# Optimization experiments

Measured on AMD Instinct MI355X. Metric: run time of the kernel, lower is better.

Reference implementation:

```python
import jax, jax.numpy as jnp
import numpy as np

NUM_SAMPLES = 100  # hard-coded in the original forward


def _bilinear(img, x, y):
    """Bilinear sample img (H,W) at pixel coords x,y (any shape); border padding.
    Matches F.grid_sample(align_corners=True, padding_mode='border') since the
    original normalizes by (W-1)/(H-1) which maps back to the same pixel coords."""
    H, W = img.shape
    x0 = jnp.floor(x); y0 = jnp.floor(y)
    wx = x - x0; wy = y - y0
    x0i = jnp.clip(x0, 0, W - 1).astype(jnp.int32)
    x1i = jnp.clip(x0 + 1, 0, W - 1).astype(jnp.int32)
    y0i = jnp.clip(y0, 0, H - 1).astype(jnp.int32)
    y1i = jnp.clip(y0 + 1, 0, H - 1).astype(jnp.int32)
    return (img[y0i, x0i] * (1 - wx) * (1 - wy)
            + img[y0i, x1i] * wx * (1 - wy)
            + img[y1i, x0i] * (1 - wx) * wy
            + img[y1i, x1i] * wx * wy)


def setup_inputs() -> dict:
    key = jax.random.key(0)
    k1, k2, k3 = jax.random.split(key, 3)
    H = W = 2048
    N = 100000
    distance_image = jax.random.uniform(k1, (H, W), dtype=jnp.float32)
    points = jax.random.uniform(k2, (N, 2), dtype=jnp.float32) * (H - 1)
    normals = jax.random.normal(k3, (N, 2), dtype=jnp.float32)
    return {"distance_image": distance_image, "points": points, "normals": normals}


def reference(distance_image, points, normals):
    H, W = distance_image.shape
    N = points.shape[0]
    # original clamps both coords to [0, max(H-1, W-1)]
    pts = jnp.clip(points, 0.0, float(max(H - 1, W - 1)))  # (N,2)

    # direction perpendicular to normal, normalized
    d = jnp.stack([-normals[:, 1], normals[:, 0]], axis=-1)
    d = d / jnp.linalg.norm(d, axis=-1, keepdims=True)  # (N,2)
    dx, dy = d[:, 0], d[:, 1]
    px, py = pts[:, 0], pts[:, 1]

    maxf = jnp.finfo(d.dtype).max
    sdx = jnp.where(dx != 0, dx, 1.0)
    sdy = jnp.where(dy != 0, dy, 1.0)
    t_left = jnp.where(dx != 0, (0.0 - px) / sdx, -maxf)
    t_right = jnp.where(dx != 0, (W - 1.0 - px) / sdx, maxf)
    t_top = jnp.where(dy != 0, (0.0 - py) / sdy, -maxf)
    t_bottom = jnp.where(dy != 0, (H - 1.0 - py) / sdy, maxf)
    t_min = jnp.maximum(t_left, t_top)
    t_max = jnp.minimum(t_right, t_bottom)

    p1 = pts + t_min[:, None] * d  # (N,2)
    p2 = pts + t_max[:, None] * d  # (N,2)

    ts = jnp.linspace(0.0, 1.0, NUM_SAMPLES, dtype=pts.dtype)  # (S,)
    line = p1[:, None, :] + ts[None, :, None] * (p2 - p1)[:, None, :]  # (N,S,2)
    lx = jnp.clip(line[..., 0], 0.0, W - 1.0)
    ly = jnp.clip(line[..., 1], 0.0, H - 1.0)
    line = jnp.stack([lx, ly], axis=-1)  # clamped sampled points (N,S,2)

    vals = _bilinear(distance_image, lx, ly)  # (N,S)
    ref_val = _bilinear(distance_image, px, py)  # (N,)

    # local minima: strict minimum vs both neighbors, indices shifted by +1
    center = vals[:, 1:-1]
    minima = (center < vals[:, :-2]) & (center < vals[:, 2:])  # (N,S-2)

    # distance from each candidate (interior sample points) to the reference point
    dist = jnp.linalg.norm(line[:, 1:-1, :] - pts[:, None, :], axis=-1)  # (N,S-2)
    dist = jnp.where(minima, dist, jnp.inf)
    nearest = jnp.argmin(dist, axis=1)  # (N,)
    nearest_val = vals[jnp.arange(N), nearest + 1]  # (N,)

    # per-point mse of two scalars, then mean over points
    return jnp.mean((nearest_val - ref_val) ** 2)
```

## Files before the change

kernel.cpp:

```cpp
#include <hip/hip_runtime.h>
#include <float.h>
#include <math.h>

#define NSAMP 100
#define IMG_W 2048
#define IMG_H 2048
#define SEG 25
#define NSEG 4
#define NREG 8

typedef _Float16 h2_t __attribute__((ext_vector_type(2), aligned(4)));
typedef _Float16 h4_t __attribute__((ext_vector_type(4), aligned(8)));
typedef _Float16 h8_t __attribute__((ext_vector_type(8), aligned(16)));

__device__ __forceinline__ float tparam(int s) {
    return (s == NSAMP - 1) ? 1.0f : (float)((double)s * (1.0 / 99.0));
}

__device__ __forceinline__ void chord(float px, float py, float nx, float ny,
                                      float& p1x, float& p1y, float& vx, float& vy) {
    float ddx = -ny, ddy = nx;
    float nrm = sqrtf(ddx * ddx + ddy * ddy);
    float dx = ddx / nrm, dy = ddy / nrm;
    const float maxf = FLT_MAX;
    float sdx = (dx != 0.f) ? dx : 1.f;
    float sdy = (dy != 0.f) ? dy : 1.f;
    float t_left   = (dx != 0.f) ? (0.f    - px) / sdx : -maxf;
    float t_right  = (dx != 0.f) ? (2047.f - px) / sdx :  maxf;
    float t_top    = (dy != 0.f) ? (0.f    - py) / sdy : -maxf;
    float t_bottom = (dy != 0.f) ? (2047.f - py) / sdy :  maxf;
    float t_min = fmaxf(t_left, t_top);
    float t_max = fminf(t_right, t_bottom);
    p1x = px + t_min * dx; p1y = py + t_min * dy;
    float p2x = px + t_max * dx, p2y = py + t_max * dy;
    vx = p2x - p1x; vy = p2y - p1y;
}

__global__ void zero_qcnt_kernel(unsigned int* __restrict__ qcnt) {
    if (threadIdx.x < NREG) qcnt[threadIdx.x] = 0u;
}

__global__ __launch_bounds__(256) void convert_bin_kernel(
        const float* __restrict__ in, h2_t* __restrict__ V,
        const float* __restrict__ points, const float* __restrict__ normals,
        float4* __restrict__ pts4, unsigned int* __restrict__ regs,
        unsigned int* __restrict__ qcnt,
        double* __restrict__ accum, unsigned int* __restrict__ done,
        int N) {
    __shared__ unsigned int lh[NREG];
    if (threadIdx.x < NREG) lh[threadIdx.x] = 0u;
    __syncthreads();
    int idx = blockIdx.x * blockDim.x + threadIdx.x;
    if (idx == 0) { *accum = 0.0; *done = 0u; }

    {
        int y  = idx >> 9;
        int x4 = (idx & 511) << 2;
        int y1 = min(y + 1, IMG_H - 1);
        float4 a = *(const float4*)(in + (size_t)y  * IMG_W + x4);
        float4 b = *(const float4*)(in + (size_t)y1 * IMG_W + x4);
        h8_t o;
        o[0] = (_Float16)a.x; o[1] = (_Float16)b.x;
        o[2] = (_Float16)a.y; o[3] = (_Float16)b.y;
        o[4] = (_Float16)a.z; o[5] = (_Float16)b.z;
        o[6] = (_Float16)a.w; o[7] = (_Float16)b.w;
        *(h8_t*)(V + (size_t)y * IMG_W + x4) = o;
    }

    if (idx < N) {
        float px = fminf(fmaxf(points[2 * idx],     0.f), 2047.f);
        float py = fminf(fmaxf(points[2 * idx + 1], 0.f), 2047.f);
        float nx = normals[2 * idx];
        float ny = normals[2 * idx + 1];
        pts4[idx] = make_float4(px, py, nx, ny);
        float p1x, p1y, vx, vy;
        chord(px, py, nx, ny, p1x, p1y, vx, vy);
        unsigned int packed = 0;
        #pragma unroll
        for (int seg = 0; seg < NSEG; ++seg) {
            int s_begin = SEG * seg;
            int s_end   = min(s_begin + SEG + 1, NSAMP - 1);
            float f = (float)(s_begin + s_end) * 0.5f / 99.0f;
            float mx = fminf(fmaxf(p1x + f * vx, 0.f), 2047.f);
            float my = fminf(fmaxf(p1y + f * vy, 0.f), 2047.f);
            unsigned int r = ((unsigned int)my >> 10) * 4u + ((unsigned int)mx >> 9);
            packed |= r << (8 * seg);
            atomicAdd(&lh[r], 1u);
        }
        regs[idx] = packed;
    }
    __syncthreads();
    if (threadIdx.x < NREG && lh[threadIdx.x]) atomicAdd(&qcnt[threadIdx.x], lh[threadIdx.x]);
}

__global__ void scan_kernel(const unsigned int* __restrict__ qcnt,
                            unsigned int* __restrict__ segoff,
                            unsigned int* __restrict__ cursor) {
    if (threadIdx.x == 0) {
        unsigned int run = 0;
        for (int r = 0; r < NREG; ++r) {
            segoff[r] = run;
            cursor[r] = run;
            run += qcnt[r];
        }
    }
}

__global__ __launch_bounds__(256) void scatter_kernel(const unsigned int* __restrict__ regs,
                                                      unsigned int* __restrict__ cursor,
                                                      unsigned int* __restrict__ seglist,
                                                      int N) {
    __shared__ unsigned int lh[NREG];
    __shared__ unsigned int lbase[NREG];
    if (threadIdx.x < NREG) lh[threadIdx.x] = 0u;
    __syncthreads();
    int i = blockIdx.x * blockDim.x + threadIdx.x;
    unsigned int packed = 0, rank[NSEG];
    if (i < N) {
        packed = regs[i];
        #pragma unroll
        for (int seg = 0; seg < NSEG; ++seg) {
            unsigned int r = (packed >> (8 * seg)) & 0xFFu;
            rank[seg] = atomicAdd(&lh[r], 1u);
        }
    }
    __syncthreads();
    if (threadIdx.x < NREG)
        lbase[threadIdx.x] = lh[threadIdx.x] ? atomicAdd(&cursor[threadIdx.x], lh[threadIdx.x]) : 0u;
    __syncthreads();
    if (i < N) {
        #pragma unroll
        for (int seg = 0; seg < NSEG; ++seg) {
            unsigned int r = (packed >> (8 * seg)) & 0xFFu;
            seglist[lbase[r] + rank[seg]] = (unsigned int)(i * 4 + seg);
        }
    }
}

__device__ __forceinline__ float bilinV(const h2_t* __restrict__ V, float x, float y) {
    float x0f = floorf(x), y0f = floorf(y);
    float wx = x - x0f, wy = y - y0f;
    int x0 = (int)x0f;
    int y0 = (int)y0f;
    int xa = min(x0, IMG_W - 2);
    bool edge = (x0 == IMG_W - 1);
    h4_t q = *(const h4_t*)(V + (size_t)y0 * IMG_W + xa);
    float v00 = edge ? (float)q[2] : (float)q[0];
    float v10 = edge ? (float)q[3] : (float)q[1];
    float v01 = (float)q[2];
    float v11 = (float)q[3];
    return v00 * (1.f - wx) * (1.f - wy) + v01 * wx * (1.f - wy)
         + v10 * (1.f - wx) * wy       + v11 * wx * wy;
}

__global__ __launch_bounds__(256) void contour_seg_kernel(
        const h2_t* __restrict__ V,
        const float4* __restrict__ pts4,
        const unsigned int* __restrict__ seglist,
        const unsigned int* __restrict__ segoff,
        const unsigned int* __restrict__ qcnt,
        float4* __restrict__ rec) {
    unsigned int q     = (unsigned int)blockIdx.x & 7u;
    unsigned int slice = (unsigned int)blockIdx.x >> 3;
    unsigned int qn = qcnt[q];
    unsigned int qo = segoff[q];
    unsigned int per = (qn + 255u) >> 8;
    unsigned int jb = slice * per;
    unsigned int je = min(jb + per, qn);

    for (unsigned int j = jb + threadIdx.x; j < je; j += 256u) {
        unsigned int e = seglist[qo + j];
        int i   = (int)(e >> 2);
        int seg = (int)(e & 3u);
        float4 pt = pts4[i];
        float px = pt.x, py = pt.y;
        float p1x, p1y, vx, vy;
        chord(px, py, pt.z, pt.w, p1x, p1y, vx, vy);

        float ref_val = 0.f;
        if (seg == 0) ref_val = bilinV(V, px, py);

        int s_begin = SEG * seg;
        int s_end   = min(s_begin + SEG + 1, NSAMP - 1);

        float tt = tparam(s_begin);
        float lx = fminf(fmaxf(p1x + tt * vx, 0.f), 2047.f);
        float ly = fminf(fmaxf(p1y + tt * vy, 0.f), 2047.f);
        float v_im1 = bilinV(V, lx, ly);
        tt = tparam(s_begin + 1);
        lx = fminf(fmaxf(p1x + tt * vx, 0.f), 2047.f);
        ly = fminf(fmaxf(p1y + tt * vy, 0.f), 2047.f);
        float v_i = bilinV(V, lx, ly);
        float cx = lx, cy = ly;

        float best_d2  = INFINITY;
        float best_idx = 1.0e9f;
        float best_val = 0.f;
        if (seg == 0) {
            best_idx = 0.f;
            best_val = v_i;
        }

        #pragma unroll 5
        for (int s = s_begin + 2; s <= s_end; ++s) {
            float ts = tparam(s);
            float nlx = fminf(fmaxf(p1x + ts * vx, 0.f), 2047.f);
            float nly = fminf(fmaxf(p1y + ts * vy, 0.f), 2047.f);
            float v_ip1 = bilinV(V, nlx, nly);
            if (v_i < v_im1 && v_i < v_ip1) {
                float ex = cx - px, ey = cy - py;
                float d2 = ex * ex + ey * ey;
                if (d2 < best_d2) { best_d2 = d2; best_idx = (float)(s - 1); best_val = v_i; }
            }
            v_im1 = v_i; v_i = v_ip1; cx = nlx; cy = nly;
        }
        rec[e] = make_float4(best_d2, best_idx, best_val, ref_val);
    }
}

__global__ __launch_bounds__(256) void reduce_kernel(const float4* __restrict__ rec,
                                                     double* __restrict__ accum,
                                                     unsigned int* __restrict__ done,
                                                     float* __restrict__ out,
                                                     int N, int nblocks) {
    int i = blockIdx.x * blockDim.x + threadIdx.x;
    float sq = 0.f;
    if (i < N) {
        float4 best = rec[4 * i];
        float ref = best.w;
        #pragma unroll
        for (int k = 1; k < NSEG; ++k) {
            float4 r = rec[4 * i + k];
            if (r.x < best.x || (r.x == best.x && r.y < best.y)) best = r;
        }
        float diff = best.z - ref;
        sq = diff * diff;
    }
    for (int off = 32; off > 0; off >>= 1)
        sq += __shfl_down(sq, off);
    __shared__ float wsum[4];
    int lane = threadIdx.x & 63;
    int wid  = threadIdx.x >> 6;
    if (lane == 0) wsum[wid] = sq;
    __syncthreads();
    if (threadIdx.x == 0) {
        float bs = wsum[0] + wsum[1] + wsum[2] + wsum[3];
        atomicAdd(accum, (double)bs);
        __threadfence();
        unsigned int prev = atomicAdd(done, 1u);
        if (prev == (unsigned int)(nblocks - 1)) {
            double total = atomicAdd(accum, 0.0);
            out[0] = (float)(total / (double)N);
        }
    }
}

extern "C" void kernel_launch(void* const* d_in, const int* in_sizes, int n_in,
                              void* d_out, int out_size, void* d_ws, size_t ws_size,
                              hipStream_t stream) {
    const float* img     = (const float*)d_in[0];
    const float* points  = (const float*)d_in[1];
    const float* normals = (const float*)d_in[2];
    int N = in_sizes[1] / 2;
    float* out = (float*)d_out;

    char* ws = (char*)d_ws;
    h2_t* V = (h2_t*)ws;
    size_t off = (size_t)IMG_W * IMG_H * sizeof(h2_t);
    double* accum        = (double*)(ws + off);       off += 8;
    unsigned int* done   = (unsigned int*)(ws + off); off += 8;
    unsigned int* qcnt   = (unsigned int*)(ws + off); off += NREG * 4;
    unsigned int* segoff = (unsigned int*)(ws + off); off += NREG * 4;
    unsigned int* cursor = (unsigned int*)(ws + off); off += NREG * 4;
    off = (off + 15) & ~(size_t)15;
    float4* pts4         = (float4*)(ws + off);       off += (size_t)N * 16;
    unsigned int* regs   = (unsigned int*)(ws + off); off += (size_t)N * 4;
    unsigned int* seglist= (unsigned int*)(ws + off); off += (size_t)N * NSEG * 4;
    off = (off + 15) & ~(size_t)15;
    float4* rec          = (float4*)(ws + off);

    zero_qcnt_kernel<<<1, 64, 0, stream>>>(qcnt);

    int conv_blocks = (IMG_W * IMG_H / 4) / 256;
    convert_bin_kernel<<<conv_blocks, 256, 0, stream>>>(img, V, points, normals,
                                                        pts4, regs, qcnt, accum, done, N);

    scan_kernel<<<1, 64, 0, stream>>>(qcnt, segoff, cursor);

    int pgrid = (N + 255) / 256;
    scatter_kernel<<<pgrid, 256, 0, stream>>>(regs, cursor, seglist, N);

    contour_seg_kernel<<<2048, 256, 0, stream>>>(V, pts4, seglist, segoff, qcnt, rec);

    reduce_kernel<<<pgrid, 256, 0, stream>>>(rec, accum, done, out, N, pgrid);
}
```

Before: 139.4 us.

## Bin line segments by region, angle and offset for coherent gathers

Segments were previously bucketed only by coarse image region. They are now sorted by a finer key: region, line angle bin and perpendicular-offset bin, built with a global histogram, a parallel scan and atomic scatter. Neighbouring threads then sample nearly parallel, nearby lines, which should improve cache locality of the bilinear gathers. The point data is also copied into sorted order so it can be read contiguously. The cost is a larger histogram, global atomics on 8192 bins during scatter, extra scatter writes, and an atan2 per point.

```diff
diff --git a/kernel.cpp b/kernel.cpp
--- a/kernel.cpp
+++ b/kernel.cpp
@@ -8,6 +8,9 @@
 #define SEG 25
 #define NSEG 4
 #define NREG 8
+#define NTB 32
+#define NRB 32
+#define NB (NREG * NTB * NRB)
 
 typedef _Float16 h2_t __attribute__((ext_vector_type(2), aligned(4)));
 typedef _Float16 h4_t __attribute__((ext_vector_type(4), aligned(8)));
@@ -36,20 +39,13 @@
     vx = p2x - p1x; vy = p2y - p1y;
 }
 
-__global__ void zero_qcnt_kernel(unsigned int* __restrict__ qcnt) {
-    if (threadIdx.x < NREG) qcnt[threadIdx.x] = 0u;
-}
-
 __global__ __launch_bounds__(256) void convert_bin_kernel(
         const float* __restrict__ in, h2_t* __restrict__ V,
         const float* __restrict__ points, const float* __restrict__ normals,
-        float4* __restrict__ pts4, unsigned int* __restrict__ regs,
-        unsigned int* __restrict__ qcnt,
+        float4* __restrict__ pts4, unsigned short* __restrict__ keys,
+        unsigned int* __restrict__ hist,
         double* __restrict__ accum, unsigned int* __restrict__ done,
         int N) {
-    __shared__ unsigned int lh[NREG];
-    if (threadIdx.x < NREG) lh[threadIdx.x] = 0u;
-    __syncthreads();
     int idx = blockIdx.x * blockDim.x + threadIdx.x;
     if (idx == 0) { *accum = 0.0; *done = 0u; }
 
@@ -75,7 +71,14 @@
         pts4[idx] = make_float4(px, py, nx, ny);
         float p1x, p1y, vx, vy;
         chord(px, py, nx, ny, p1x, p1y, vx, vy);
-        unsigned int packed = 0;
+
+        float ddx = -ny, ddy = nx;
+        float nrm = sqrtf(ddx * ddx + ddy * ddy);
+        float dx = ddx / nrm, dy = ddy / nrm;
+        if (dy < 0.f || (dy == 0.f && dx < 0.f)) { dx = -dx; dy = -dy; }
+        float theta = atan2f(dy, dx);
+        int tb = min(max((int)(theta * ((float)NTB / 3.14159274f)), 0), NTB - 1);
+
         #pragma unroll
         for (int seg = 0; seg < NSEG; ++seg) {
             int s_begin = SEG * seg;
@@ -84,56 +87,65 @@
             float mx = fminf(fmaxf(p1x + f * vx, 0.f), 2047.f);
             float my = fminf(fmaxf(p1y + f * vy, 0.f), 2047.f);
             unsigned int r = ((unsigned int)my >> 10) * 4u + ((unsigned int)mx >> 9);
-            packed |= r << (8 * seg);
-            atomicAdd(&lh[r], 1u);
-        }
-        regs[idx] = packed;
-    }
+            float rcx = (float)((r & 3u) * 512u + 256u);
+            float rcy = (float)((r >> 2) * 1024u + 512u);
+            float rho = (px - rcx) * (-dy) + (py - rcy) * dx;
+            int rb = min(max((int)((rho + 572.4f) * ((float)NRB / 1144.8f)), 0), NRB - 1);
+            unsigned int key = (r << 10) | ((unsigned int)tb << 5) | (unsigned int)rb;
+            keys[idx * NSEG + seg] = (unsigned short)key;
+            atomicAdd(&hist[key], 1u);
+        }
+    }
+}
+
+__global__ __launch_bounds__(256) void scan_kernel(const unsigned int* __restrict__ hist,
+                                                   unsigned int* __restrict__ cursor,
+                                                   unsigned int* __restrict__ segoff8,
+                                                   unsigned int* __restrict__ qcnt8) {
+    __shared__ unsigned int s[256];
+    int t = threadIdx.x;
+    int base = t * (NB / 256);
+    unsigned int sum = 0;
+    for (int k = 0; k < NB / 256; ++k) sum += hist[base + k];
+    s[t] = sum;
     __syncthreads();
-    if (threadIdx.x < NREG && lh[threadIdx.x]) atomicAdd(&qcnt[threadIdx.x], lh[threadIdx.x]);
-}
-
-__global__ void scan_kernel(const unsigned int* __restrict__ qcnt,
-                            unsigned int* __restrict__ segoff,
-                            unsigned int* __restrict__ cursor) {
-    if (threadIdx.x == 0) {
-        unsigned int run = 0;
+    for (int off = 1; off < 256; off <<= 1) {
+        unsigned int v = (t >= off) ? s[t - off] : 0u;
+        __syncthreads();
+        s[t] += v;
+        __syncthreads();
+    }
+    unsigned int run = (t == 0) ? 0u : s[t - 1];
+    for (int k = 0; k < NB / 256; ++k) {
+        cursor[base + k] = run;
+        run += hist[base + k];
+    }
+    __syncthreads();
+    if (t == 0) {
         for (int r = 0; r < NREG; ++r) {
-            segoff[r] = run;
-            cursor[r] = run;
-            run += qcnt[r];
-        }
-    }
-}
-
-__global__ __launch_bounds__(256) void scatter_kernel(const unsigned int* __restrict__ regs,
+            unsigned int lo = (r == 0) ? 0u : s[r * 32 - 1];
+            unsigned int hi = s[(r + 1) * 32 - 1];
+            segoff8[r] = lo;
+            qcnt8[r]  = hi - lo;
+        }
+    }
+}
+
+__global__ __launch_bounds__(256) void scatter_kernel(const unsigned short* __restrict__ keys,
+                                                      const float4* __restrict__ pts4,
                                                       unsigned int* __restrict__ cursor,
-                                                      unsigned int* __restrict__ seglist,
+                                                      unsigned int* __restrict__ se,
+                                                      float4* __restrict__ spt,
                                                       int N) {
-    __shared__ unsigned int lh[NREG];
-    __shared__ unsigned int lbase[NREG];
-    if (threadIdx.x < NREG) lh[threadIdx.x] = 0u;
-    __syncthreads();
     int i = blockIdx.x * blockDim.x + threadIdx.x;
-    unsigned int packed = 0, rank[NSEG];
-    if (i < N) {
-        packed = regs[i];
-        #pragma unroll
-        for (int seg = 0; seg < NSEG; ++seg) {
-            unsigned int r = (packed >> (8 * seg)) & 0xFFu;
-            rank[seg] = atomicAdd(&lh[r], 1u);
-        }
-    }
-    __syncthreads();
-    if (threadIdx.x < NREG)
-        lbase[threadIdx.x] = lh[threadIdx.x] ? atomicAdd(&cursor[threadIdx.x], lh[threadIdx.x]) : 0u;
-    __syncthreads();
-    if (i < N) {
-        #pragma unroll
-        for (int seg = 0; seg < NSEG; ++seg) {
-            unsigned int r = (packed >> (8 * seg)) & 0xFFu;
-            seglist[lbase[r] + rank[seg]] = (unsigned int)(i * 4 + seg);
-        }
+    if (i >= N) return;
+    float4 pt = pts4[i];
+    #pragma unroll
+    for (int seg = 0; seg < NSEG; ++seg) {
+        unsigned int key = keys[i * NSEG + seg];
+        unsigned int pos = atomicAdd(&cursor[key], 1u);
+        se[pos]  = (unsigned int)(i * NSEG + seg);
+        spt[pos] = pt;
     }
 }
 
@@ -155,24 +167,23 @@
 
 __global__ __launch_bounds__(256) void contour_seg_kernel(
         const h2_t* __restrict__ V,
-        const float4* __restrict__ pts4,
-        const unsigned int* __restrict__ seglist,
-        const unsigned int* __restrict__ segoff,
-        const unsigned int* __restrict__ qcnt,
+        const float4* __restrict__ spt,
+        const unsigned int* __restrict__ se,
+        const unsigned int* __restrict__ segoff8,
+        const unsigned int* __restrict__ qcnt8,
         float4* __restrict__ rec) {
     unsigned int q     = (unsigned int)blockIdx.x & 7u;
     unsigned int slice = (unsigned int)blockIdx.x >> 3;
-    unsigned int qn = qcnt[q];
-    unsigned int qo = segoff[q];
+    unsigned int qn = qcnt8[q];
+    unsigned int qo = segoff8[q];
     unsigned int per = (qn + 255u) >> 8;
     unsigned int jb = slice * per;
     unsigned int je = min(jb + per, qn);
 
     for (unsigned int j = jb + threadIdx.x; j < je; j += 256u) {
-        unsigned int e = seglist[qo + j];
-        int i   = (int)(e >> 2);
+        unsigned int e = se[qo + j];
         int seg = (int)(e & 3u);
-        float4 pt = pts4[i];
+        float4 pt = spt[qo + j];
         float px = pt.x, py = pt.y;
         float p1x, p1y, vx, vy;
         chord(px, py, pt.z, pt.w, p1x, p1y, vx, vy);
@@ -267,30 +278,33 @@
     char* ws = (char*)d_ws;
     h2_t* V = (h2_t*)ws;
     size_t off = (size_t)IMG_W * IMG_H * sizeof(h2_t);
-    double* accum        = (double*)(ws + off);       off += 8;
-    unsigned int* done   = (unsigned int*)(ws + off); off += 8;
-    unsigned int* qcnt   = (unsigned int*)(ws + off); off += NREG * 4;
-    unsigned int* segoff = (unsigned int*)(ws + off); off += NREG * 4;
-    unsigned int* cursor = (unsigned int*)(ws + off); off += NREG * 4;
+    double* accum          = (double*)(ws + off);       off += 8;
+    unsigned int* done     = (unsigned int*)(ws + off); off += 8;
+    unsigned int* hist     = (unsigned int*)(ws + off); off += (size_t)NB * 4;
+    unsigned int* cursor   = (unsigned int*)(ws + off); off += (size_t)NB * 4;
+    unsigned int* segoff8  = (unsigned int*)(ws + off); off += NREG * 4;
+    unsigned int* qcnt8    = (unsigned int*)(ws + off); off += NREG * 4;
     off = (off + 15) & ~(size_t)15;
-    float4* pts4         = (float4*)(ws + off);       off += (size_t)N * 16;
-    unsigned int* regs   = (unsigned int*)(ws + off); off += (size_t)N * 4;
-    unsigned int* seglist= (unsigned int*)(ws + off); off += (size_t)N * NSEG * 4;
+    float4* pts4           = (float4*)(ws + off);       off += (size_t)N * 16;
+    unsigned short* keys   = (unsigned short*)(ws + off); off += (size_t)N * NSEG * 2;
+    off = (off + 3) & ~(size_t)3;
+    unsigned int* se       = (unsigned int*)(ws + off); off += (size_t)N * NSEG * 4;
     off = (off + 15) & ~(size_t)15;
-    float4* rec          = (float4*)(ws + off);
-
-    zero_qcnt_kernel<<<1, 64, 0, stream>>>(qcnt);
+    float4* spt            = (float4*)(ws + off);       off += (size_t)N * NSEG * 16;
+    float4* rec            = (float4*)(ws + off);
+
+    hipMemsetAsync(hist, 0, (size_t)NB * 4, stream);
 
     int conv_blocks = (IMG_W * IMG_H / 4) / 256;
     convert_bin_kernel<<<conv_blocks, 256, 0, stream>>>(img, V, points, normals,
-                                                        pts4, regs, qcnt, accum, done, N);
-
-    scan_kernel<<<1, 64, 0, stream>>>(qcnt, segoff, cursor);
+                                                        pts4, keys, hist, accum, done, N);
+
+    scan_kernel<<<1, 256, 0, stream>>>(hist, cursor, segoff8, qcnt8);
 
     int pgrid = (N + 255) / 256;
-    scatter_kernel<<<pgrid, 256, 0, stream>>>(regs, cursor, seglist, N);
-
-    contour_seg_kernel<<<2048, 256, 0, stream>>>(V, pts4, seglist, segoff, qcnt, rec);
+    scatter_kernel<<<pgrid, 256, 0, stream>>>(keys, pts4, cursor, se, spt, N);
+
+    contour_seg_kernel<<<2048, 256, 0, stream>>>(V, spt, se, segoff8, qcnt8, rec);
 
     reduce_kernel<<<pgrid, 256, 0, stream>>>(rec, accum, done, out, N, pgrid);
 }
```

After: 198.8 us. 1.43x slower.
